# Kernel optimization log

Measured on AMD Instinct MI355X. Metric: run time of the kernel, lower is better.

Reference implementation:

```python
import jax, jax.numpy as jnp
import numpy as np

R_CHK, N_VAR, BATCH, ITERS, NLEV, ROW_DEG = 144, 576, 512, 3, 16, 15


def setup_inputs() -> dict:
    key = jax.random.key(0)
    rng = np.random.default_rng(0)
    Hnp = np.zeros((R_CHK, N_VAR), np.float32)
    cols = np.argsort(rng.random((R_CHK, N_VAR)), axis=1)[:, :ROW_DEG]
    Hnp[np.arange(R_CHK)[:, None], cols] = 1.0
    H = jnp.asarray(Hnp)
    r = jax.random.normal(key, (BATCH, N_VAR), jnp.float32) * 2.0  # channel LLRs
    alpha = jnp.full((ITERS,), 0.7, jnp.float32)
    beta = jnp.full((ITERS,), 0.05, jnp.float32)
    eta = jnp.full((ITERS,), 0.7, jnp.float32)
    qk = jnp.linspace(-4.0, 4.0, NLEV).astype(jnp.float32)  # learned codebook
    return {"r": r, "alpha": alpha, "beta": beta, "eta": eta, "qk": qk, "H": H}


def _c_to_v(M, alpha, beta, Hb):
    # Normalized offset min-sum check-node update, excluding self-message.
    mag = jnp.where(Hb, jnp.abs(M), jnp.inf)              # [B,R,C]
    two = -jax.lax.top_k(-mag, 2)[0]                      # two smallest per row
    m1, m2 = two[..., 0:1], two[..., 1:2]
    min_excl = jnp.where(mag == m1, m2, m1)               # min over other edges
    sgn = jnp.where(Hb, jnp.sign(M), 1.0)
    row_sign = jnp.prod(sgn, axis=-1, keepdims=True)
    E = alpha * row_sign * sgn * jnp.maximum(min_excl - beta, 0.0)
    return jnp.where(Hb, E, 0.0)


def _quantize(x, eta, qk):
    # Nearest-level lookup in sorted codebook qk, applied to eta*x.
    bnd = 0.5 * (qk[:-1] + qk[1:])                        # [NLEV-1] midpoints
    idx = jnp.searchsorted(bnd, eta * x)
    return qk[idx]


def _decode(r, alpha, beta, eta, qk, H):
    Hb = H > 0.5                                          # [R,C] edge mask
    M = H[None] * r[:, None, :]                           # initial_M: [B,R,C]
    E = jnp.zeros_like(M)
    for it in range(ITERS):
        E = _c_to_v(M, alpha[it], beta[it], Hb)
        E = _quantize(E, eta[it], qk) * H                 # Q on check messages
        col = jnp.sum(E, axis=1, keepdims=True)           # [B,1,C]
        M = H[None] * (r[:, None, :] + col - E)           # update_M (extrinsic)
        M = _quantize(M, eta[it], qk) * H                 # Q on var messages
    return r + jnp.sum(E, axis=1)                         # [B,C]


def reference(r, alpha, beta, eta, qk, H):
    return _decode(r, alpha, beta, eta, qk, H)
```

## Files before the change

### kernel.cpp

```cpp
#include <hip/hip_runtime.h>
#include <hip/hip_bf16.h>
#include <math.h>

#define R_CHK   144
#define N_VAR   576
#define BATCH   512
#define ITERS   3
#define NLEV    16
#define ROW_DEG 15
#define N_EDGE  (R_CHK * ROW_DEG)
#define NWORDS  9

__launch_bounds__(64)
__global__ void k1_bitmask(const float* __restrict__ H,
                           unsigned long long* __restrict__ bits,
                           int* __restrict__ edge_cols) {
    const int i    = blockIdx.x;
    const int lane = threadIdx.x;

    float h[NWORDS];
#pragma unroll
    for (int s = 0; s < NWORDS; ++s) h[s] = H[i * N_VAR + s * 64 + lane];

    unsigned long long m[NWORDS];
#pragma unroll
    for (int s = 0; s < NWORDS; ++s) m[s] = __ballot(h[s] > 0.5f);

#pragma unroll
    for (int s = 0; s < NWORDS; ++s)
        if (lane == s) bits[i * NWORDS + s] = m[s];

    if (lane == 0) {
        int k = 0;
#pragma unroll
        for (int s = 0; s < NWORDS; ++s) {
            unsigned long long mm = m[s];
            while (mm) {
                int b = __ffsll((long long)mm) - 1;
                if (k < ROW_DEG) edge_cols[i * ROW_DEG + k] = s * 64 + b;
                ++k;
                mm &= mm - 1;
            }
        }
    }
}

__launch_bounds__(N_VAR)
__global__ void k2_csr(const unsigned long long* __restrict__ bits,
                       int* __restrict__ col_ptr,
                       int* __restrict__ col_csr) {
    __shared__ unsigned long long sb[R_CHK * NWORDS];
    __shared__ int spref[R_CHK * NWORDS];
    __shared__ int sscan[2][N_VAR];

    const int t = threadIdx.x;

    for (int e = t; e < R_CHK * NWORDS; e += N_VAR) sb[e] = bits[e];
    __syncthreads();

    for (int idx = t; idx < R_CHK * NWORDS; idx += N_VAR) {
        int i = idx / NWORDS, w = idx % NWORDS;
        int p = 0;
        for (int u = 0; u < w; ++u) p += __popcll(sb[i * NWORDS + u]);
        spref[idx] = p;
    }

    const int w   = t >> 6;
    const int bit = t & 63;
    const unsigned long long vmask   = 1ull << bit;
    const unsigned long long lowmask = vmask - 1ull;
    int n = 0;
    for (int i0 = 0; i0 < R_CHK; i0 += 16) {
        unsigned long long mw[16];
#pragma unroll
        for (int j = 0; j < 16; ++j) mw[j] = sb[(i0 + j) * NWORDS + w];
#pragma unroll
        for (int j = 0; j < 16; ++j) n += (int)((mw[j] >> bit) & 1ull);
    }
    __syncthreads();
    sscan[0][t] = n;
    __syncthreads();

    int src = 0;
    for (int off = 1; off < N_VAR; off <<= 1) {
        int v = sscan[src][t];
        if (t >= off) v += sscan[src][t - off];
        sscan[src ^ 1][t] = v;
        src ^= 1;
        __syncthreads();
    }

    const int myptr = sscan[src][t] - n;
    col_ptr[t] = myptr;
    if (t == N_VAR - 1) col_ptr[N_VAR] = sscan[src][t];

    int p = myptr;
    for (int i0 = 0; i0 < R_CHK; i0 += 16) {
        unsigned long long mw[16];
        int pf[16];
#pragma unroll
        for (int j = 0; j < 16; ++j) {
            mw[j] = sb[(i0 + j) * NWORDS + w];
            pf[j] = spref[(i0 + j) * NWORDS + w];
        }
#pragma unroll
        for (int j = 0; j < 16; ++j) {
            if (mw[j] & vmask) {
                int rank = pf[j] + __popcll(mw[j] & lowmask);
                col_csr[p++] = (i0 + j) * ROW_DEG + rank;
            }
        }
    }
}

__launch_bounds__(256)
__global__ void decode_kernel(const float* __restrict__ r,
                              const float* __restrict__ alpha,
                              const float* __restrict__ beta,
                              const float* __restrict__ eta,
                              const float* __restrict__ qk,
                              const int* __restrict__ edge_cols,
                              const int* __restrict__ col_ptr,
                              const int* __restrict__ col_csr,
                              float* __restrict__ out) {
    __shared__ float sE[N_EDGE];
    __shared__ float sr[N_VAR];
    __shared__ float st[N_VAR];
    __shared__ int   s_csr[N_EDGE];
    __shared__ int   s_ptr[N_VAR + 1];

    const int b = blockIdx.x;
    const int t = threadIdx.x;

    const float qv = qk[t & 15];
    float bnd[NLEV - 1];
#pragma unroll
    for (int j = 0; j < NLEV - 1; ++j) bnd[j] = 0.5f * (qk[j] + qk[j + 1]);

    float av[ITERS], bv[ITERS], ev[ITERS];
#pragma unroll
    for (int i = 0; i < ITERS; ++i) { av[i] = alpha[i]; bv[i] = beta[i]; ev[i] = eta[i]; }

    for (int e = t; e < N_EDGE; e += 256) s_csr[e] = col_csr[e];
    for (int v = t; v < N_VAR + 1; v += 256) s_ptr[v] = col_ptr[v];
    for (int v = t; v < N_VAR; v += 256) sr[v] = r[b * N_VAR + v];

    const bool isrow = (t < R_CHK);
    int cols[ROW_DEG];
    if (isrow) {
#pragma unroll
        for (int k = 0; k < ROW_DEG; ++k) cols[k] = edge_cols[t * ROW_DEG + k];
    }
    __syncthreads();

    float M[ROW_DEG], Eq[ROW_DEG];
    if (isrow) {
#pragma unroll
        for (int k = 0; k < ROW_DEG; ++k) M[k] = sr[cols[k]];
    }

#pragma unroll
    for (int it = 0; it < ITERS; ++it) {
        const float a   = av[it];
        const float bta = bv[it];
        const float et  = ev[it];

        if (isrow) {
            if (it > 0) {
                const float etp = ev[it - 1];
#pragma unroll
                for (int k = 0; k < ROW_DEG; ++k) {
                    float x = st[cols[k]] - Eq[k];
                    float y = etp * x;
                    int idx = 0;
#pragma unroll
                    for (int j = 0; j < NLEV - 1; ++j) idx += (y > bnd[j]) ? 1 : 0;
                    M[k] = __shfl(qv, idx);
                }
            }

            float m1 = INFINITY, m2 = INFINITY;
            float prod = 1.0f;
#pragma unroll
            for (int k = 0; k < ROW_DEG; ++k) {
                float ab = fabsf(M[k]);
                if (ab < m1)      { m2 = m1; m1 = ab; }
                else if (ab < m2) { m2 = ab; }
                float s = (M[k] > 0.0f) ? 1.0f : ((M[k] < 0.0f) ? -1.0f : 0.0f);
                prod *= s;
            }
#pragma unroll
            for (int k = 0; k < ROW_DEG; ++k) {
                float ab = fabsf(M[k]);
                float mexcl = (ab == m1) ? m2 : m1;
                float s  = (M[k] > 0.0f) ? 1.0f : ((M[k] < 0.0f) ? -1.0f : 0.0f);
                float E  = ((a * prod) * s) * fmaxf(mexcl - bta, 0.0f);
                float y = et * E;
                int idx = 0;
#pragma unroll
                for (int j = 0; j < NLEV - 1; ++j) idx += (y > bnd[j]) ? 1 : 0;
                float eq = __shfl(qv, idx);
                Eq[k] = eq;
                sE[t * ROW_DEG + k] = eq;
            }
        }
        __syncthreads();

        for (int v = t; v < N_VAR; v += 256) {
            float sum = 0.0f;
            const int p0 = s_ptr[v], p1 = s_ptr[v + 1];
            for (int j = p0; j < p1; ++j) sum += sE[s_csr[j]];
            float stv = sr[v] + sum;
            st[v] = stv;
            if (it == ITERS - 1) out[b * N_VAR + v] = stv;
        }
        if (it < ITERS - 1) __syncthreads();
    }
}

extern "C" void kernel_launch(void* const* d_in, const int* in_sizes, int n_in,
                              void* d_out, int out_size, void* d_ws, size_t ws_size,
                              hipStream_t stream) {
    const float* r     = (const float*)d_in[0];
    const float* alpha = (const float*)d_in[1];
    const float* beta  = (const float*)d_in[2];
    const float* eta   = (const float*)d_in[3];
    const float* qk    = (const float*)d_in[4];
    const float* H     = (const float*)d_in[5];
    float* out = (float*)d_out;

    unsigned long long* bits = (unsigned long long*)d_ws;
    int* edge_cols = (int*)(bits + R_CHK * NWORDS);
    int* col_ptr   = edge_cols + N_EDGE;
    int* col_csr   = col_ptr + (N_VAR + 1);

    k1_bitmask<<<R_CHK, 64, 0, stream>>>(H, bits, edge_cols);
    k2_csr<<<1, N_VAR, 0, stream>>>(bits, col_ptr, col_csr);
    decode_kernel<<<BATCH, 256, 0, stream>>>(r, alpha, beta, eta, qk,
                                             edge_cols, col_ptr, col_csr, out);
}
```

Measured before the change: 50.86 us.

## Merge index kernels and spread check-node work across four lanes per row

```diff
diff --git a/kernel.cpp b/kernel.cpp
--- a/kernel.cpp
+++ b/kernel.cpp
@@ -10,209 +10,212 @@
 #define ROW_DEG 15
 #define N_EDGE  (R_CHK * ROW_DEG)
 #define NWORDS  9
-
-__launch_bounds__(64)
-__global__ void k1_bitmask(const float* __restrict__ H,
-                           unsigned long long* __restrict__ bits,
-                           int* __restrict__ edge_cols) {
-    const int i    = blockIdx.x;
-    const int lane = threadIdx.x;
-
-    float h[NWORDS];
-#pragma unroll
-    for (int s = 0; s < NWORDS; ++s) h[s] = H[i * N_VAR + s * 64 + lane];
-
-    unsigned long long m[NWORDS];
-#pragma unroll
-    for (int s = 0; s < NWORDS; ++s) m[s] = __ballot(h[s] > 0.5f);
-
-#pragma unroll
-    for (int s = 0; s < NWORDS; ++s)
-        if (lane == s) bits[i * NWORDS + s] = m[s];
-
-    if (lane == 0) {
-        int k = 0;
-#pragma unroll
-        for (int s = 0; s < NWORDS; ++s) {
-            unsigned long long mm = m[s];
-            while (mm) {
-                int b = __ffsll((long long)mm) - 1;
-                if (k < ROW_DEG) edge_cols[i * ROW_DEG + k] = s * 64 + b;
-                ++k;
-                mm &= mm - 1;
-            }
-        }
-    }
-}
-
-__launch_bounds__(N_VAR)
-__global__ void k2_csr(const unsigned long long* __restrict__ bits,
-                       int* __restrict__ col_ptr,
-                       int* __restrict__ col_csr) {
+#define DEG_PAD 16
+#define SLOT    16
+#define NTHR    576
+
+__launch_bounds__(NTHR)
+__global__ void k12_index(const float* __restrict__ H,
+                          int* __restrict__ edge_cols,
+                          unsigned short* __restrict__ col_pack) {
     __shared__ unsigned long long sb[R_CHK * NWORDS];
     __shared__ int spref[R_CHK * NWORDS];
-    __shared__ int sscan[2][N_VAR];
-
-    const int t = threadIdx.x;
-
-    for (int e = t; e < R_CHK * NWORDS; e += N_VAR) sb[e] = bits[e];
+
+    const int t    = threadIdx.x;
+    const int w    = t >> 6;
+    const int lane = t & 63;
+
+    for (int j0 = 0; j0 < 16; j0 += 4) {
+        float h[4][NWORDS];
+#pragma unroll
+        for (int jj = 0; jj < 4; ++jj)
+#pragma unroll
+            for (int s = 0; s < NWORDS; ++s)
+                h[jj][s] = H[(16 * w + j0 + jj) * N_VAR + s * 64 + lane];
+#pragma unroll
+        for (int jj = 0; jj < 4; ++jj)
+#pragma unroll
+            for (int s = 0; s < NWORDS; ++s) {
+                unsigned long long m = __ballot(h[jj][s] > 0.5f);
+                if (lane == s) sb[(16 * w + j0 + jj) * NWORDS + s] = m;
+            }
+    }
     __syncthreads();
 
-    for (int idx = t; idx < R_CHK * NWORDS; idx += N_VAR) {
-        int i = idx / NWORDS, w = idx % NWORDS;
-        int p = 0;
-        for (int u = 0; u < w; ++u) p += __popcll(sb[i * NWORDS + u]);
-        spref[idx] = p;
-    }
-
-    const int w   = t >> 6;
-    const int bit = t & 63;
-    const unsigned long long vmask   = 1ull << bit;
-    const unsigned long long lowmask = vmask - 1ull;
-    int n = 0;
-    for (int i0 = 0; i0 < R_CHK; i0 += 16) {
-        unsigned long long mw[16];
-#pragma unroll
-        for (int j = 0; j < 16; ++j) mw[j] = sb[(i0 + j) * NWORDS + w];
-#pragma unroll
-        for (int j = 0; j < 16; ++j) n += (int)((mw[j] >> bit) & 1ull);
+    if (t < R_CHK) {
+        int k = 0, p = 0;
+#pragma unroll
+        for (int s = 0; s < NWORDS; ++s) {
+            unsigned long long m = sb[t * NWORDS + s];
+            spref[t * NWORDS + s] = p;
+            p += __popcll(m);
+            while (m) {
+                int bpos = __ffsll((long long)m) - 1;
+                if (k < ROW_DEG) edge_cols[t * ROW_DEG + k] = s * 64 + bpos;
+                ++k;
+                m &= m - 1;
+            }
+        }
     }
     __syncthreads();
-    sscan[0][t] = n;
-    __syncthreads();
-
-    int src = 0;
-    for (int off = 1; off < N_VAR; off <<= 1) {
-        int v = sscan[src][t];
-        if (t >= off) v += sscan[src][t - off];
-        sscan[src ^ 1][t] = v;
-        src ^= 1;
-        __syncthreads();
-    }
-
-    const int myptr = sscan[src][t] - n;
-    col_ptr[t] = myptr;
-    if (t == N_VAR - 1) col_ptr[N_VAR] = sscan[src][t];
-
-    int p = myptr;
-    for (int i0 = 0; i0 < R_CHK; i0 += 16) {
-        unsigned long long mw[16];
-        int pf[16];
-#pragma unroll
-        for (int j = 0; j < 16; ++j) {
-            mw[j] = sb[(i0 + j) * NWORDS + w];
-            pf[j] = spref[(i0 + j) * NWORDS + w];
-        }
-#pragma unroll
-        for (int j = 0; j < 16; ++j) {
-            if (mw[j] & vmask) {
-                int rank = pf[j] + __popcll(mw[j] & lowmask);
-                col_csr[p++] = (i0 + j) * ROW_DEG + rank;
-            }
-        }
+
+    {
+        const int wq  = t >> 6;
+        const int bit = t & 63;
+        const unsigned long long vmask   = 1ull << bit;
+        const unsigned long long lowmask = vmask - 1ull;
+        int n = 0;
+        for (int i0 = 0; i0 < R_CHK; i0 += 16) {
+            unsigned long long mw[16];
+            int pf[16];
+#pragma unroll
+            for (int j = 0; j < 16; ++j) {
+                mw[j] = sb[(i0 + j) * NWORDS + wq];
+                pf[j] = spref[(i0 + j) * NWORDS + wq];
+            }
+#pragma unroll
+            for (int j = 0; j < 16; ++j) {
+                if (mw[j] & vmask) {
+                    int rank = pf[j] + __popcll(mw[j] & lowmask);
+                    if (n < DEG_PAD)
+                        col_pack[t * DEG_PAD + n] =
+                            (unsigned short)((i0 + j) * SLOT + rank);
+                    ++n;
+                }
+            }
+        }
+        for (int j = (n < DEG_PAD ? n : DEG_PAD); j < DEG_PAD; ++j)
+            col_pack[t * DEG_PAD + j] = 15;
     }
 }
 
-__launch_bounds__(256)
+__launch_bounds__(NTHR, 5)
 __global__ void decode_kernel(const float* __restrict__ r,
                               const float* __restrict__ alpha,
                               const float* __restrict__ beta,
                               const float* __restrict__ eta,
-                              const float* __restrict__ qk,
+                              const float* __restrict__ qkg,
                               const int* __restrict__ edge_cols,
-                              const int* __restrict__ col_ptr,
-                              const int* __restrict__ col_csr,
+                              const int* __restrict__ col_pack,
                               float* __restrict__ out) {
-    __shared__ float sE[N_EDGE];
-    __shared__ float sr[N_VAR];
+    __shared__ float sE[R_CHK * SLOT];
     __shared__ float st[N_VAR];
-    __shared__ int   s_csr[N_EDGE];
-    __shared__ int   s_ptr[N_VAR + 1];
-
-    const int b = blockIdx.x;
-    const int t = threadIdx.x;
-
-    const float qv = qk[t & 15];
+
+    const int b   = blockIdx.x;
+    const int t   = threadIdx.x;
+    const int row = t >> 2;
+    const int g   = t & 3;
+
+    const float qv = qkg[t & 15];
     float bnd[NLEV - 1];
 #pragma unroll
-    for (int j = 0; j < NLEV - 1; ++j) bnd[j] = 0.5f * (qk[j] + qk[j + 1]);
+    for (int j = 0; j < NLEV - 1; ++j) bnd[j] = 0.5f * (qkg[j] + qkg[j + 1]);
+    auto QI = [&](float y) -> int {
+        int idx = 0;
+#pragma unroll
+        for (int j = 0; j < NLEV - 1; ++j) idx += (y > bnd[j]) ? 1 : 0;
+        return idx;
+    };
+    const float q0 = __shfl(qv, QI(0.0f));
 
     float av[ITERS], bv[ITERS], ev[ITERS];
 #pragma unroll
     for (int i = 0; i < ITERS; ++i) { av[i] = alpha[i]; bv[i] = beta[i]; ev[i] = eta[i]; }
 
-    for (int e = t; e < N_EDGE; e += 256) s_csr[e] = col_csr[e];
-    for (int v = t; v < N_VAR + 1; v += 256) s_ptr[v] = col_ptr[v];
-    for (int v = t; v < N_VAR; v += 256) sr[v] = r[b * N_VAR + v];
-
-    const bool isrow = (t < R_CHK);
-    int cols[ROW_DEG];
-    if (isrow) {
-#pragma unroll
-        for (int k = 0; k < ROW_DEG; ++k) cols[k] = edge_cols[t * ROW_DEG + k];
-    }
+    int pp[8];
+    {
+        const int4* p4 = (const int4*)col_pack + t * 2;
+        int4 a0 = p4[0], a1 = p4[1];
+        pp[0] = a0.x; pp[1] = a0.y; pp[2] = a0.z; pp[3] = a0.w;
+        pp[4] = a1.x; pp[5] = a1.y; pp[6] = a1.z; pp[7] = a1.w;
+    }
+
+    int cols[4];
+#pragma unroll
+    for (int j = 0; j < 4; ++j) {
+        const int ke = 4 * g + j;
+        cols[j] = (ke < ROW_DEG) ? edge_cols[row * ROW_DEG + ke] : 0;
+    }
+
+    const float rv = r[b * N_VAR + t];
+    st[t] = rv;
     __syncthreads();
 
-    float M[ROW_DEG], Eq[ROW_DEG];
-    if (isrow) {
-#pragma unroll
-        for (int k = 0; k < ROW_DEG; ++k) M[k] = sr[cols[k]];
-    }
+    float M[4], Eq[4];
+#pragma unroll
+    for (int j = 0; j < 4; ++j) M[j] = st[cols[j]];
 
 #pragma unroll
     for (int it = 0; it < ITERS; ++it) {
-        const float a   = av[it];
-        const float bta = bv[it];
-        const float et  = ev[it];
-
-        if (isrow) {
-            if (it > 0) {
-                const float etp = ev[it - 1];
-#pragma unroll
-                for (int k = 0; k < ROW_DEG; ++k) {
-                    float x = st[cols[k]] - Eq[k];
-                    float y = etp * x;
-                    int idx = 0;
-#pragma unroll
-                    for (int j = 0; j < NLEV - 1; ++j) idx += (y > bnd[j]) ? 1 : 0;
-                    M[k] = __shfl(qv, idx);
-                }
-            }
-
-            float m1 = INFINITY, m2 = INFINITY;
-            float prod = 1.0f;
-#pragma unroll
-            for (int k = 0; k < ROW_DEG; ++k) {
-                float ab = fabsf(M[k]);
-                if (ab < m1)      { m2 = m1; m1 = ab; }
-                else if (ab < m2) { m2 = ab; }
-                float s = (M[k] > 0.0f) ? 1.0f : ((M[k] < 0.0f) ? -1.0f : 0.0f);
-                prod *= s;
-            }
-#pragma unroll
-            for (int k = 0; k < ROW_DEG; ++k) {
-                float ab = fabsf(M[k]);
-                float mexcl = (ab == m1) ? m2 : m1;
-                float s  = (M[k] > 0.0f) ? 1.0f : ((M[k] < 0.0f) ? -1.0f : 0.0f);
-                float E  = ((a * prod) * s) * fmaxf(mexcl - bta, 0.0f);
-                float y = et * E;
-                int idx = 0;
-#pragma unroll
-                for (int j = 0; j < NLEV - 1; ++j) idx += (y > bnd[j]) ? 1 : 0;
-                float eq = __shfl(qv, idx);
-                Eq[k] = eq;
-                sE[t * ROW_DEG + k] = eq;
-            }
+        const float a = av[it], bta = bv[it], et = ev[it];
+
+        if (it > 0) {
+            const float etp = ev[it - 1];
+#pragma unroll
+            for (int j = 0; j < 4; ++j) {
+                float x = st[cols[j]] - Eq[j];
+                M[j] = __shfl(qv, QI(etp * x));
+            }
+        }
+
+        float sg[4], ab[4];
+#pragma unroll
+        for (int j = 0; j < 4; ++j) {
+            const int ke = 4 * g + j;
+            float m = M[j];
+            float s = (m > 0.0f) ? 1.0f : ((m < 0.0f) ? -1.0f : 0.0f);
+            sg[j] = (ke < ROW_DEG) ? s : 1.0f;
+            ab[j] = (ke < ROW_DEG) ? fabsf(m) : INFINITY;
+        }
+        float pl = (sg[0] * sg[1]) * (sg[2] * sg[3]);
+        float l1a = fminf(ab[0], ab[1]), l2a = fmaxf(ab[0], ab[1]);
+        float l1b = fminf(ab[2], ab[3]), l2b = fmaxf(ab[2], ab[3]);
+        float m1 = fminf(l1a, l1b);
+        float m2 = fminf(fmaxf(l1a, l1b), fminf(l2a, l2b));
+        {
+            float o1 = __shfl_xor(m1, 1), o2 = __shfl_xor(m2, 1);
+            float n1 = fminf(m1, o1);
+            float n2 = fminf(fmaxf(m1, o1), fminf(m2, o2));
+            m1 = n1; m2 = n2;
+            float op = __shfl_xor(pl, 1); pl *= op;
+            o1 = __shfl_xor(m1, 2); o2 = __shfl_xor(m2, 2);
+            n1 = fminf(m1, o1);
+            n2 = fminf(fmaxf(m1, o1), fminf(m2, o2));
+            m1 = n1; m2 = n2;
+            op = __shfl_xor(pl, 2); pl *= op;
+        }
+
+        const float ap = a * pl;
+        const float g1 = fmaxf(m1 - bta, 0.0f);
+        const float g2 = fmaxf(m2 - bta, 0.0f);
+        const float y1 = et * (ap * g1);
+        const float y2 = et * (ap * g2);
+        const float c1p = __shfl(qv, QI(y1)), c1m = __shfl(qv, QI(-y1));
+        const float c2p = __shfl(qv, QI(y2)), c2m = __shfl(qv, QI(-y2));
+#pragma unroll
+        for (int j = 0; j < 4; ++j) {
+            const int ke = 4 * g + j;
+            const bool ismin = (ab[j] == m1);
+            float cp = ismin ? c2p : c1p;
+            float cm = ismin ? c2m : c1m;
+            float q = (sg[j] > 0.0f) ? cp : cm;
+            q = (sg[j] == 0.0f) ? q0 : q;
+            q = (ke < ROW_DEG) ? q : 0.0f;
+            Eq[j] = q;
+            sE[row * SLOT + ke] = q;
         }
         __syncthreads();
 
-        for (int v = t; v < N_VAR; v += 256) {
-            float sum = 0.0f;
-            const int p0 = s_ptr[v], p1 = s_ptr[v + 1];
-            for (int j = p0; j < p1; ++j) sum += sE[s_csr[j]];
-            float stv = sr[v] + sum;
-            st[v] = stv;
-            if (it == ITERS - 1) out[b * N_VAR + v] = stv;
+        {
+            float s = 0.0f;
+#pragma unroll
+            for (int j = 0; j < DEG_PAD; ++j) {
+                int id = (pp[j >> 1] >> (16 * (j & 1))) & 0xffff;
+                s += sE[id];
+            }
+            float stv = rv + s;
+            st[t] = stv;
+            if (it == ITERS - 1) out[b * N_VAR + t] = stv;
         }
         if (it < ITERS - 1) __syncthreads();
     }
@@ -229,13 +232,10 @@
     const float* H     = (const float*)d_in[5];
     float* out = (float*)d_out;
 
-    unsigned long long* bits = (unsigned long long*)d_ws;
-    int* edge_cols = (int*)(bits + R_CHK * NWORDS);
-    int* col_ptr   = edge_cols + N_EDGE;
-    int* col_csr   = col_ptr + (N_VAR + 1);
-
-    k1_bitmask<<<R_CHK, 64, 0, stream>>>(H, bits, edge_cols);
-    k2_csr<<<1, N_VAR, 0, stream>>>(bits, col_ptr, col_csr);
-    decode_kernel<<<BATCH, 256, 0, stream>>>(r, alpha, beta, eta, qk,
-                                             edge_cols, col_ptr, col_csr, out);
+    int* edge_cols = (int*)d_ws;
+    unsigned short* col_pack = (unsigned short*)(edge_cols + N_EDGE);
+
+    k12_index<<<1, NTHR, 0, stream>>>(H, edge_cols, col_pack);
+    decode_kernel<<<BATCH, NTHR, 0, stream>>>(r, alpha, beta, eta, qk,
+                                              edge_cols, (const int*)col_pack, out);
 }
```

After: 40.97 us. -19.5%, faster.
